# Kernel tuning notes

Measured on AMD Instinct MI355X. Metric: run time of the kernel, lower is better.

Reference implementation:

```python
import math
import numpy as np
import jax, jax.numpy as jnp

LMAX1, LMAX2 = 10, 5
F1, F2 = 20, 40
B_IN, B_L1, B_L2 = 96, 10, 6
ASPECT = 2
BATCH = 32
ACT_CST = math.sqrt(2.0)  # normalize2mom(relu): E[relu(z)^2]=1/2 for z~N(0,1)


def _fact(n):
    return float(math.factorial(n))


def wigner_d_small(l, beta):
    # Wigner small-d matrices, complex-m ordering m=-l..l -> [n, 2l+1, 2l+1]
    beta = np.asarray(beta, dtype=np.float64)
    n = beta.shape[0]
    d = np.zeros((n, 2 * l + 1, 2 * l + 1))
    c, s = np.cos(beta / 2), np.sin(beta / 2)
    for imp, mp in enumerate(range(-l, l + 1)):
        for im, m in enumerate(range(-l, l + 1)):
            pref = math.sqrt(_fact(l + mp) * _fact(l - mp) * _fact(l + m) * _fact(l - m))
            val = np.zeros(n)
            for k in range(max(0, m - mp), min(l + m, l - mp) + 1):
                den = _fact(l + m - k) * _fact(k) * _fact(mp - m + k) * _fact(l - mp - k)
                val += (-1.0) ** (mp - m + k) / den * c ** (2 * l + m - mp - 2 * k) * s ** (mp - m + 2 * k)
            d[:, imp, im] = pref * val
    return d


def U_c2r(l):
    # unitary change of basis complex SH -> real SH, Yr = U @ Yc
    U = np.zeros((2 * l + 1, 2 * l + 1), dtype=np.complex128)
    U[l, l] = 1.0
    sq = 1.0 / math.sqrt(2.0)
    for m in range(1, l + 1):
        cs = (-1.0) ** m
        U[l + m, l + m] = cs * sq
        U[l + m, l - m] = sq
        U[l - m, l + m] = -1j * cs * sq
        U[l - m, l - m] = 1j * sq
    return U


def rot_z_real(l, ang):
    # real-basis rotation about the azimuthal axis -> [n, 2l+1, 2l+1]
    U = U_c2r(l)
    m = np.arange(-l, l + 1)
    ph = np.exp(-1j * np.outer(np.asarray(ang, np.float64), m))
    return np.real(np.einsum('ik,nk,jk->nij', U, ph, U.conj(), optimize=True))


def d_real(l, beta):
    U = U_c2r(l)
    dc = wigner_d_small(l, beta).astype(np.complex128)
    return np.real(np.einsum('ij,njk,lk->nil', U, dc, U.conj(), optimize=True))


def wigner_D_pts(l, a, b, g):
    return np.einsum('nij,njk,nkm->nim', rot_z_real(l, a), d_real(l, b), rot_z_real(l, g), optimize=True)


def flat_wigner_pts(lmax, a, b, g):
    n = len(a)
    return np.concatenate([math.sqrt(2 * l + 1) * wigner_D_pts(l, a, b, g).reshape(n, -1) for l in range(lmax + 1)], -1)


def flat_wigner_grid(lmax, al, be, ga):
    # product grid (alpha x beta x gamma), flattened alpha-major -> [na*nb*ng, sum (2l+1)^2]
    blocks = []
    for l in range(lmax + 1):
        D = np.einsum('aij,bjk,gkm->abgim', rot_z_real(l, al), d_real(l, be), rot_z_real(l, ga), optimize=True)
        blocks.append(math.sqrt(2 * l + 1) * D.reshape(-1, (2 * l + 1) ** 2))
    return np.concatenate(blocks, -1)


def sh_pts(lmax, a, b):
    # component-normalized real SH at points: Y_l = sqrt(2l+1) * D^l(a,b,0)[:, m=0]
    cols = []
    for l in range(lmax + 1):
        M = np.einsum('nij,nj->ni', rot_z_real(l, a), d_real(l, b)[:, :, l], optimize=True)
        cols.append(math.sqrt(2 * l + 1) * M)
    return np.concatenate(cols, -1)


def sh_grid(lmax, al, be):
    # SH on product grid, flattened beta-major to match x.transpose(-1,-2) layout
    cols = []
    for l in range(lmax + 1):
        M = np.einsum('aij,bj->bai', rot_z_real(l, al), d_real(l, be)[:, :, l], optimize=True)
        cols.append(math.sqrt(2 * l + 1) * M.reshape(-1, 2 * l + 1))
    return np.concatenate(cols, -1)


def _so3_grid(res):
    nb, na = 2 * res, 2 * res * ASPECT
    al = 2 * math.pi * np.arange(na) / na
    be = math.pi * (np.arange(nb) + 0.5) / nb
    return al, be, al.copy()


def setup_inputs():
    key = jax.random.key(0)
    k1, k2, k3 = jax.random.split(key, 3)
    # kernel grids (near identity), as in s2/so3_near_identity_grid
    b_s2 = np.arange(1, 4) * (math.pi / 8) / 3
    a_s2 = np.linspace(0, 2 * math.pi, 9)[:-1]
    ga, gb = np.meshgrid(a_s2, b_s2, indexing='ij')
    Yk1 = sh_pts(LMAX1, ga.ravel(), gb.ravel())  # [24, 121]
    a_so3 = np.linspace(0, 2 * math.pi, 8)[:-1]
    g_so3 = np.linspace(-2 * math.pi, 2 * math.pi, 8)
    ga, gb, gg = np.meshgrid(a_so3, b_s2, g_so3, indexing='ij')
    Dk2 = flat_wigner_pts(LMAX2, ga.ravel(), gb.ravel(), gg.ravel())  # [168, 286]
    # FromS2Grid analysis matrix (pinv of band-limited synthesis matrix)
    be = (np.arange(B_IN) + 0.5) / B_IN * math.pi
    al = np.arange(B_IN) / B_IN * 2 * math.pi
    from_s2 = np.linalg.pinv(sh_grid(LMAX1, al, be))  # [121, 9216]
    # SO(3) activation transform matrices
    a1, b1, g1 = _so3_grid(B_L1)
    D1_to = flat_wigner_grid(LMAX1, a1, b1, g1)                     # [32000, 1771]
    F1_from = np.linalg.pinv(flat_wigner_grid(LMAX2, a1, b1, g1))   # [286, 32000]
    a2, b2, g2 = _so3_grid(B_L2)
    D2_to = flat_wigner_grid(LMAX2, a2, b2, g2)                     # [6912, 286]
    F2_from = np.linalg.pinv(flat_wigner_grid(0, a2, b2, g2))       # [1, 6912]
    f32 = lambda v: jnp.asarray(v, dtype=jnp.float32)
    return {
        'x': jax.random.normal(k1, (BATCH, 1, B_IN, B_IN), dtype=jnp.float32),
        'w1': jax.random.normal(k2, (1, F1, Yk1.shape[0]), dtype=jnp.float32),
        'w2': jax.random.normal(k3, (F1, F2, Dk2.shape[0]), dtype=jnp.float32),
        'Yk1': f32(Yk1), 'Dk2': f32(Dk2), 'from_s2': f32(from_s2),
        'D1_to': f32(D1_to), 'F1_from': f32(F1_from),
        'D2_to': f32(D2_to), 'F2_from': f32(F2_from),
    }


def reference(x, w1, w2, Yk1, Dk2, from_s2, D1_to, F1_from, D2_to, F2_from):
    B = x.shape[0]
    # [B,1,alpha,beta] -> [B,1,beta,alpha] -> S2 Fourier coefficients
    c = jnp.einsum('bfg,cg->bfc', jnp.swapaxes(x, -1, -2).reshape(B, 1, -1), from_s2)  # [B,1,121]
    # S2 -> SO(3) convolution (e3nn Linear with SH-built weights)
    psi1 = jnp.einsum('ni,xyn->xyi', Yk1, w1) / math.sqrt(Yk1.shape[0])  # [1,F1,121]
    outs = []
    for l in range(LMAX1 + 1):
        k = 2 * l + 1
        ol = jnp.einsum('bim,ijn->bjnm', c[:, :, l * l:l * l + k], psi1[:, :, l * l:l * l + k])  # fan_in = 1
        outs.append(ol.reshape(B, F1, k * k))
    h = jnp.concatenate(outs, -1)  # [B,F1,1771]
    # SO(3) activation: Fourier -> grid, relu, grid -> Fourier (lmax 10 -> 5)
    g = ACT_CST * jax.nn.relu(jnp.einsum('bfc,gc->bfg', h, D1_to))
    h = jnp.einsum('bfg,cg->bfc', g, F1_from)  # [B,F1,286]
    # SO(3) -> SO(3) convolution (Wigner-D-built weights)
    psi2 = jnp.einsum('nc,xyn->xyc', Dk2, w2) / math.sqrt(Dk2.shape[0])  # [F1,F2,286]
    outs, off = [], 0
    for l in range(LMAX2 + 1):
        k = 2 * l + 1
        xl = h[:, :, off:off + k * k].reshape(B, F1, k, k)       # [B,i,u,m]
        pl = psi2[:, :, off:off + k * k].reshape(F1, F2, k, k)   # [i,j,u,v]
        ol = jnp.einsum('bium,ijuv->bjvm', xl, pl) / math.sqrt(F1 * k)  # fan_in = F1*(2l+1)
        outs.append(ol.reshape(B, F2, k * k))
        off += k * k
    h = jnp.concatenate(outs, -1)  # [B,F2,286]
    # final SO(3) activation lmax 5 -> 0
    g = ACT_CST * jax.nn.relu(jnp.einsum('bfc,gc->bfg', h, D2_to))
    return jnp.einsum('bfg,cg->bfc', g, F2_from)  # [B,F2,1]
```

## Files before the change

kernel.cpp:

```cpp
#include <hip/hip_runtime.h>
#include <hip/hip_bf16.h>
#include <math.h>


#define B_      32
#define F1_     20
#define F2_     40
#define NC1     1771
#define K1P     1792
#define NG1     32000
#define NC2     286
#define K2P     288
#define NG2     6912
#define SQRT2_  1.41421356237309515f
#define RS24    0.20412414523193154f
#define RS168   0.07715167498104595f

typedef unsigned int   uint32;
typedef unsigned short u16;
typedef __attribute__((ext_vector_type(8))) short short8;
typedef __attribute__((ext_vector_type(4))) float f32x4;

#define AS1(p) ((const __attribute__((address_space(1))) void*)(p))
#define AS3(p) ((__attribute__((address_space(3))) void*)(p))

__device__ __forceinline__ u16 f2bf(float f) {
  uint32 u = __float_as_uint(f);
  return (u16)((u + 0x7FFFu + ((u >> 16) & 1u)) >> 16);
}
__device__ __forceinline__ uint32 pack_bf16(float lo, float hi) {
  uint32 a = __float_as_uint(lo), b = __float_as_uint(hi);
  a = (a + 0x7FFFu + ((a >> 16) & 1u)) >> 16;
  b = (b + 0x7FFFu + ((b >> 16) & 1u)) & 0xFFFF0000u;
  return a | b;
}

__device__ __forceinline__ float wave_reduce(float v) {
#pragma unroll
  for (int o = 32; o > 0; o >>= 1) v += __shfl_down(v, o, 64);
  return v;
}


__global__ void k_c(const float* __restrict__ x, const float* __restrict__ fs,
                    float* __restrict__ c) {
  const int ch = blockIdx.x, b = blockIdx.y, tid = threadIdx.x;
  const float* xb = x + b * 9216;
  const float* fr = fs + ch * 9216;
  float s = 0.f;
  for (int g = tid; g < 9216; g += 256) {
    s += xb[(g % 96) * 96 + (g / 96)] * fr[g];
  }
  s = wave_reduce(s);
  __shared__ float red[4];
  if ((tid & 63) == 0) red[tid >> 6] = s;
  __syncthreads();
  if (tid == 0) c[b * 121 + ch] = red[0] + red[1] + red[2] + red[3];
}

__global__ void k_psi1(const float* __restrict__ Yk1, const float* __restrict__ w1,
                       float* __restrict__ psi1) {
  const int j = blockIdx.x, i = threadIdx.x;
  __shared__ float wsm[24];
  if (i < 24) wsm[i] = w1[j * 24 + i];
  __syncthreads();
  if (i < 121) {
    float s = 0.f;
#pragma unroll
    for (int n = 0; n < 24; ++n) s += Yk1[n * 121 + i] * wsm[n];
    psi1[j * 121 + i] = s * RS24;
  }
}

__global__ void k_h(const float* __restrict__ c, const float* __restrict__ psi1,
                    u16* __restrict__ hb) {
  const int j = blockIdx.x, b = blockIdx.y, tid = threadIdx.x;
  __shared__ float cs[121], ps[121];
  if (tid < 121) { cs[tid] = c[b * 121 + tid]; ps[tid] = psi1[j * 121 + tid]; }
  __syncthreads();
  for (int idx = tid; idx < K1P; idx += 256) {
    u16 v = 0;
    if (idx < NC1) {
      int off = 0, l = 0, k = 1;
      while (idx >= off + k * k) { off += k * k; ++l; k += 2; }
      const int r = idx - off, n = r / k, m = r % k;
      v = f2bf(cs[l * l + m] * ps[l * l + n]);
    }
    hb[(size_t)(b * F1_ + j) * K1P + idx] = v;
  }
}


__global__ void k_cvt1(const float* __restrict__ in, uint32* __restrict__ out) {
  const int total = 32000 * 896;
  for (int id = blockIdx.x * 256 + threadIdx.x; id < total; id += gridDim.x * 256) {
    const int r = id / 896, c2 = id % 896, cc = c2 * 2;
    const float* p = in + (size_t)r * NC1 + cc;
    const float lo = (cc < NC1) ? p[0] : 0.f;
    const float hi = (cc + 1 < NC1) ? p[1] : 0.f;
    out[id] = pack_bf16(lo, hi);
  }
}

__global__ void k_cvt2(const float* __restrict__ in, uint32* __restrict__ out) {
  const int total = 286 * 16000;
  for (int id = blockIdx.x * 256 + threadIdx.x; id < total; id += gridDim.x * 256) {
    out[id] = pack_bf16(in[2 * id], in[2 * id + 1]);
  }
}

__global__ void k_cvt3(const float* __restrict__ in, uint32* __restrict__ out) {
  const int total = 6912 * 144;
  for (int id = blockIdx.x * 256 + threadIdx.x; id < total; id += gridDim.x * 256) {
    const int r = id / 144, c2 = id % 144, cc = c2 * 2;
    const float* p = in + (size_t)r * NC2 + cc;
    const float lo = (cc < NC2) ? p[0] : 0.f;
    const float hi = (cc + 1 < NC2) ? p[1] : 0.f;
    out[id] = pack_bf16(lo, hi);
  }
}


__launch_bounds__(256)
__global__ void k_gemm1_v3(const u16* __restrict__ A, const u16* __restrict__ B,
                           u16* __restrict__ C) {
  __shared__ __align__(16) u16 As[128 * 32];
  __shared__ __align__(16) u16 Bs[128 * 32];
  const int bid = blockIdx.x;
  const int g = bid / 40, loc = bid % 40;
  int nt, mt;
  if (g < 31) { nt = g * 8 + (loc & 7); mt = loc >> 3; }
  else        { nt = 248 + (loc & 1);  mt = loc >> 1; }
  const int m0 = mt * 128, n0 = nt * 128;
  const int tid = threadIdx.x;
  const int lane = tid & 63, w = tid >> 6;
  const int wm = w >> 1, wn = w & 1;
  const int q = lane >> 4, r16 = lane & 15;

  f32x4 acc[4][4] = {};
  const u16* ag = A + (size_t)(m0 + (tid >> 2)) * K1P + (tid & 3) * 8;
  const u16* bg = B + (size_t)(n0 + (tid >> 2)) * K1P + (tid & 3) * 8;

  for (int k0 = 0; k0 < K1P; k0 += 32) {
#pragma unroll
    for (int i = 0; i < 2; ++i) {
      __builtin_amdgcn_global_load_lds(AS1(ag + k0 + (size_t)i * 64 * K1P),
                                       AS3((char*)As + i * 4096 + w * 1024), 16, 0, 0);
      __builtin_amdgcn_global_load_lds(AS1(bg + k0 + (size_t)i * 64 * K1P),
                                       AS3((char*)Bs + i * 4096 + w * 1024), 16, 0, 0);
    }
    __syncthreads();
    short8 af[4], bf[4];
#pragma unroll
    for (int mb = 0; mb < 4; ++mb)
      af[mb] = *(const short8*)&As[(wm * 64 + mb * 16 + r16) * 32 + q * 8];
#pragma unroll
    for (int nb = 0; nb < 4; ++nb)
      bf[nb] = *(const short8*)&Bs[(wn * 64 + nb * 16 + r16) * 32 + q * 8];
#pragma unroll
    for (int mb = 0; mb < 4; ++mb)
#pragma unroll
      for (int nb = 0; nb < 4; ++nb)
        acc[mb][nb] = __builtin_amdgcn_mfma_f32_16x16x32_bf16(af[mb], bf[nb], acc[mb][nb], 0, 0, 0);
    __syncthreads();
  }
#pragma unroll
  for (int mb = 0; mb < 4; ++mb) {
#pragma unroll
    for (int nb = 0; nb < 4; ++nb) {
      const int col = n0 + wn * 64 + nb * 16 + r16;
#pragma unroll
      for (int r = 0; r < 4; ++r) {
        const int row = m0 + wm * 64 + mb * 16 + q * 4 + r;
        float v = acc[mb][nb][r];
        v = (v > 0.f) ? v * SQRT2_ : 0.f;
        C[(size_t)row * NG1 + col] = f2bf(v);
      }
    }
  }
}

__launch_bounds__(256)
__global__ void k_gemm2_v3(const u16* __restrict__ A, const u16* __restrict__ B,
                           float* __restrict__ C) {
  __shared__ __align__(16) u16 As[128 * 32];
  __shared__ __align__(16) u16 Bs[128 * 32];
  const int m0 = blockIdx.x * 128, n0 = blockIdx.y * 128;
  const int ks = blockIdx.z * 1600;
  const int tid = threadIdx.x;
  const int lane = tid & 63, w = tid >> 6;
  const int wm = w >> 1, wn = w & 1;
  const int q = lane >> 4, r16 = lane & 15;

  f32x4 acc[4][4] = {};
  const u16* ag = A + (size_t)(m0 + (tid >> 2)) * NG1 + ks + (tid & 3) * 8;
  int rb0 = n0 + (tid >> 2);        if (rb0 > 285) rb0 = 285;
  int rb1 = n0 + (tid >> 2) + 64;   if (rb1 > 285) rb1 = 285;
  const u16* bg0 = B + (size_t)rb0 * NG1 + ks + (tid & 3) * 8;
  const u16* bg1 = B + (size_t)rb1 * NG1 + ks + (tid & 3) * 8;

  for (int kt = 0; kt < 1600; kt += 32) {
#pragma unroll
    for (int i = 0; i < 2; ++i) {
      __builtin_amdgcn_global_load_lds(AS1(ag + kt + (size_t)i * 64 * NG1),
                                       AS3((char*)As + i * 4096 + w * 1024), 16, 0, 0);
    }
    __builtin_amdgcn_global_load_lds(AS1(bg0 + kt), AS3((char*)Bs + w * 1024), 16, 0, 0);
    __builtin_amdgcn_global_load_lds(AS1(bg1 + kt), AS3((char*)Bs + 4096 + w * 1024), 16, 0, 0);
    __syncthreads();
    short8 af[4], bf[4];
#pragma unroll
    for (int mb = 0; mb < 4; ++mb)
      af[mb] = *(const short8*)&As[(wm * 64 + mb * 16 + r16) * 32 + q * 8];
#pragma unroll
    for (int nb = 0; nb < 4; ++nb)
      bf[nb] = *(const short8*)&Bs[(wn * 64 + nb * 16 + r16) * 32 + q * 8];
#pragma unroll
    for (int mb = 0; mb < 4; ++mb)
#pragma unroll
      for (int nb = 0; nb < 4; ++nb)
        acc[mb][nb] = __builtin_amdgcn_mfma_f32_16x16x32_bf16(af[mb], bf[nb], acc[mb][nb], 0, 0, 0);
    __syncthreads();
  }
#pragma unroll
  for (int mb = 0; mb < 4; ++mb) {
#pragma unroll
    for (int nb = 0; nb < 4; ++nb) {
      const int col = n0 + wn * 64 + nb * 16 + r16;
      if (col < NC2) {
#pragma unroll
        for (int r = 0; r < 4; ++r) {
          const int row = m0 + wm * 64 + mb * 16 + q * 4 + r;
          atomicAdd(&C[(size_t)row * NC2 + col], acc[mb][nb][r]);
        }
      }
    }
  }
}

__launch_bounds__(256)
__global__ void k_gemm3_v3(const u16* __restrict__ A, const u16* __restrict__ B,
                           const float* __restrict__ wv, float* __restrict__ out) {
  __shared__ __align__(16) u16 As[128 * 32];
  __shared__ __align__(16) u16 Bs[128 * 32];
  __shared__ float red[128][33];
  const int m0 = blockIdx.x * 128, n0 = blockIdx.y * 128;
  const int tid = threadIdx.x;
  const int lane = tid & 63, w = tid >> 6;
  const int wm = w >> 1, wn = w & 1;
  const int q = lane >> 4, r16 = lane & 15;

  f32x4 acc[4][4] = {};
  const u16* ag = A + (size_t)(m0 + (tid >> 2)) * K2P + (tid & 3) * 8;
  const u16* bg = B + (size_t)(n0 + (tid >> 2)) * K2P + (tid & 3) * 8;

  for (int k0 = 0; k0 < K2P; k0 += 32) {
#pragma unroll
    for (int i = 0; i < 2; ++i) {
      __builtin_amdgcn_global_load_lds(AS1(ag + k0 + (size_t)i * 64 * K2P),
                                       AS3((char*)As + i * 4096 + w * 1024), 16, 0, 0);
      __builtin_amdgcn_global_load_lds(AS1(bg + k0 + (size_t)i * 64 * K2P),
                                       AS3((char*)Bs + i * 4096 + w * 1024), 16, 0, 0);
    }
    __syncthreads();
    short8 af[4], bf[4];
#pragma unroll
    for (int mb = 0; mb < 4; ++mb)
      af[mb] = *(const short8*)&As[(wm * 64 + mb * 16 + r16) * 32 + q * 8];
#pragma unroll
    for (int nb = 0; nb < 4; ++nb)
      bf[nb] = *(const short8*)&Bs[(wn * 64 + nb * 16 + r16) * 32 + q * 8];
#pragma unroll
    for (int mb = 0; mb < 4; ++mb)
#pragma unroll
      for (int nb = 0; nb < 4; ++nb)
        acc[mb][nb] = __builtin_amdgcn_mfma_f32_16x16x32_bf16(af[mb], bf[nb], acc[mb][nb], 0, 0, 0);
    __syncthreads();
  }
  float wvv[4];
#pragma unroll
  for (int nb = 0; nb < 4; ++nb) wvv[nb] = wv[n0 + wn * 64 + nb * 16 + r16];
#pragma unroll
  for (int mb = 0; mb < 4; ++mb) {
#pragma unroll
    for (int r = 0; r < 4; ++r) {
      const int rowl = wm * 64 + mb * 16 + q * 4 + r;
      float t = 0.f;
#pragma unroll
      for (int nb = 0; nb < 4; ++nb) {
        float v = acc[mb][nb][r];
        v = (v > 0.f) ? v : 0.f;
        t += v * wvv[nb];
      }
      red[rowl][wn * 16 + r16] = t;
    }
  }
  __syncthreads();
  if (tid < 128) {
    float s = 0.f;
#pragma unroll
    for (int cc = 0; cc < 32; ++cc) s += red[tid][cc];
    atomicAdd(&out[m0 + tid], s * SQRT2_);
  }
}


__launch_bounds__(256)
__global__ void k_gemm1_mfma(const u16* __restrict__ A, const float* __restrict__ Bf,
                             u16* __restrict__ C) {
  __shared__ __align__(16) u16 As[128 * 32];
  __shared__ __align__(16) u16 Bs[128 * 32];
  const int tid = threadIdx.x;
  const int lane = tid & 63, w = tid >> 6;
  const int wm = w >> 1, wn = w & 1;
  const int q = lane >> 4, r16 = lane & 15;
  const int m0 = blockIdx.x * 128, n0 = blockIdx.y * 128;

  f32x4 acc[4][4] = {};
  const u16* ag = A + (size_t)(m0 + (tid >> 2)) * K1P + (tid & 3) * 8;

  for (int k0 = 0; k0 < K1P; k0 += 32) {
#pragma unroll
    for (int i = 0; i < 2; ++i) {
      __builtin_amdgcn_global_load_lds(AS1(ag + k0 + (size_t)i * 64 * K1P),
                                       AS3((char*)As + i * 4096 + w * 1024), 16, 0, 0);
    }
#pragma unroll
    for (int i = 0; i < 8; ++i) {
      const int p = i * 256 + tid;
      const int row = p >> 4, c2 = (p & 15) * 2;
      const int kk = k0 + c2;
      const float* bp = Bf + (size_t)(n0 + row) * NC1 + kk;
      const float lo = (kk < NC1) ? bp[0] : 0.f;
      const float hi = (kk + 1 < NC1) ? bp[1] : 0.f;
      ((uint32*)Bs)[row * 16 + (p & 15)] = pack_bf16(lo, hi);
    }
    __syncthreads();
    short8 af[4], bf[4];
#pragma unroll
    for (int mb = 0; mb < 4; ++mb)
      af[mb] = *(const short8*)&As[(wm * 64 + mb * 16 + r16) * 32 + q * 8];
#pragma unroll
    for (int nb = 0; nb < 4; ++nb)
      bf[nb] = *(const short8*)&Bs[(wn * 64 + nb * 16 + r16) * 32 + q * 8];
#pragma unroll
    for (int mb = 0; mb < 4; ++mb)
#pragma unroll
      for (int nb = 0; nb < 4; ++nb)
        acc[mb][nb] = __builtin_amdgcn_mfma_f32_16x16x32_bf16(af[mb], bf[nb], acc[mb][nb], 0, 0, 0);
    __syncthreads();
  }
#pragma unroll
  for (int mb = 0; mb < 4; ++mb) {
#pragma unroll
    for (int nb = 0; nb < 4; ++nb) {
      const int col = n0 + wn * 64 + nb * 16 + r16;
#pragma unroll
      for (int r = 0; r < 4; ++r) {
        const int row = m0 + wm * 64 + mb * 16 + q * 4 + r;
        float v = acc[mb][nb][r];
        v = (v > 0.f) ? v * SQRT2_ : 0.f;
        C[(size_t)row * NG1 + col] = f2bf(v);
      }
    }
  }
}

__launch_bounds__(256)
__global__ void k_gemm2_mfma(const u16* __restrict__ A, const float* __restrict__ Bf,
                             float* __restrict__ C) {
  __shared__ __align__(16) u16 As[128 * 32];
  __shared__ __align__(16) u16 Bs[128 * 32];
  const int tid = threadIdx.x;
  const int lane = tid & 63, w = tid >> 6;
  const int wm = w >> 1, wn = w & 1;
  const int q = lane >> 4, r16 = lane & 15;
  const int m0 = blockIdx.x * 128, n0 = blockIdx.y * 128;
  const int ks = blockIdx.z * 1600;

  f32x4 acc[4][4] = {};
  const u16* ag = A + (size_t)(m0 + (tid >> 2)) * NG1 + ks + (tid & 3) * 8;

  for (int kt = 0; kt < 1600; kt += 32) {
#pragma unroll
    for (int i = 0; i < 2; ++i) {
      __builtin_amdgcn_global_load_lds(AS1(ag + kt + (size_t)i * 64 * NG1),
                                       AS3((char*)As + i * 4096 + w * 1024), 16, 0, 0);
    }
#pragma unroll
    for (int i = 0; i < 4; ++i) {
      const int idx = i * 256 + tid;
      const int row = idx >> 3, c4 = (idx & 7) * 4;
      const int n = n0 + row;
      float4 v = make_float4(0.f, 0.f, 0.f, 0.f);
      if (n < NC2) v = *(const float4*)(Bf + (size_t)n * NG1 + ks + kt + c4);
      ((uint32*)Bs)[row * 16 + (idx & 7) * 2]     = pack_bf16(v.x, v.y);
      ((uint32*)Bs)[row * 16 + (idx & 7) * 2 + 1] = pack_bf16(v.z, v.w);
    }
    __syncthreads();
    short8 af[4], bf[4];
#pragma unroll
    for (int mb = 0; mb < 4; ++mb)
      af[mb] = *(const short8*)&As[(wm * 64 + mb * 16 + r16) * 32 + q * 8];
#pragma unroll
    for (int nb = 0; nb < 4; ++nb)
      bf[nb] = *(const short8*)&Bs[(wn * 64 + nb * 16 + r16) * 32 + q * 8];
#pragma unroll
    for (int mb = 0; mb < 4; ++mb)
#pragma unroll
      for (int nb = 0; nb < 4; ++nb)
        acc[mb][nb] = __builtin_amdgcn_mfma_f32_16x16x32_bf16(af[mb], bf[nb], acc[mb][nb], 0, 0, 0);
    __syncthreads();
  }
#pragma unroll
  for (int mb = 0; mb < 4; ++mb) {
#pragma unroll
    for (int nb = 0; nb < 4; ++nb) {
      const int col = n0 + wn * 64 + nb * 16 + r16;
      if (col < NC2) {
#pragma unroll
        for (int r = 0; r < 4; ++r) {
          const int row = m0 + wm * 64 + mb * 16 + q * 4 + r;
          atomicAdd(&C[(size_t)row * NC2 + col], acc[mb][nb][r]);
        }
      }
    }
  }
}


__global__ void k_psi2(const float* __restrict__ Dk2, const float* __restrict__ w2,
                       float* __restrict__ psi2) {
  const int blk = blockIdx.x, tid = threadIdx.x;
  __shared__ float w2s[168];
  if (tid < 168) w2s[tid] = w2[blk * 168 + tid];
  __syncthreads();
  for (int cc = tid; cc < NC2; cc += 256) {
    float s = 0.f;
    for (int n = 0; n < 168; ++n) s += Dk2[n * NC2 + cc] * w2s[n];
    psi2[blk * NC2 + cc] = s * RS168;
  }
}

__global__ void k_step7(const float* __restrict__ h2, const float* __restrict__ psi2,
                        u16* __restrict__ h3b) {
  const int j = blockIdx.x, b = blockIdx.y, tid = threadIdx.x;
  __shared__ float sh[20 * 286];
  __shared__ float sp[20 * 286];
  for (int e = tid; e < 20 * 286; e += 256) {
    const int i = e / 286, cc = e % 286;
    sh[e] = h2[(b * F1_ + i) * NC2 + cc];
    sp[e] = psi2[(i * F2_ + j) * NC2 + cc];
  }
  __syncthreads();
  for (int cidx = tid; cidx < K2P; cidx += 256) {
    u16 ov = 0;
    if (cidx < NC2) {
      int off = 0, l = 0, k = 1;
      while (cidx >= off + k * k) { off += k * k; ++l; k += 2; }
      const int r = cidx - off, v = r / k, m = r % k;
      float acc = 0.f;
      for (int i = 0; i < 20; ++i) {
        const float* hbp = &sh[i * 286 + off];
        const float* pb = &sp[i * 286 + off];
        for (int u = 0; u < k; ++u) acc += hbp[u * k + m] * pb[u * k + v];
      }
      ov = f2bf(acc * rsqrtf(20.f * (float)k));
    }
    h3b[(size_t)(b * F2_ + j) * K2P + cidx] = ov;
  }
}


extern "C" void kernel_launch(void* const* d_in, const int* in_sizes, int n_in,
                              void* d_out, int out_size, void* d_ws, size_t ws_size,
                              hipStream_t stream) {
  const float* x       = (const float*)d_in[0];
  const float* w1      = (const float*)d_in[1];
  const float* w2      = (const float*)d_in[2];
  const float* Yk1     = (const float*)d_in[3];
  const float* Dk2     = (const float*)d_in[4];
  const float* from_s2 = (const float*)d_in[5];
  const float* D1_to   = (const float*)d_in[6];
  const float* F1_from = (const float*)d_in[7];
  const float* D2_to   = (const float*)d_in[8];
  const float* F2_from = (const float*)d_in[9];
  float* out = (float*)d_out;

  float* ws = (float*)d_ws;
  float* c    = ws + 0;
  float* psi1 = ws + 3872;
  float* h2   = ws + 6292;
  float* psi2 = ws + 189332;
  u16*   h3b  = (u16*)(ws + 418132);
  u16*   hb   = (u16*)(ws + 602452);
  u16*   g    = (u16*)(ws + 1175892);
  u16*   D2bf = (u16*)(ws + 11415892);
  u16*   F1bf = (u16*)(ws + 12411220);
  u16*   D1bf = (u16*)(ws + 16987220);
  const size_t BIG_NEED = (size_t)45659220 * 4;
  const bool big = ws_size >= BIG_NEED;

  k_c   <<<dim3(121, 32), 256, 0, stream>>>(x, from_s2, c);
  k_psi1<<<dim3(20),      128, 0, stream>>>(Yk1, w1, psi1);
  k_h   <<<dim3(20, 32),  256, 0, stream>>>(c, psi1, hb);
  k_cvt3<<<dim3(1024),    256, 0, stream>>>(D2_to, (uint32*)D2bf);

  if (big) {
    k_cvt1<<<dim3(8192), 256, 0, stream>>>(D1_to, (uint32*)D1bf);
    k_cvt2<<<dim3(4096), 256, 0, stream>>>(F1_from, (uint32*)F1bf);
    k_gemm1_v3<<<dim3(1250), 256, 0, stream>>>(hb, D1bf, g);
    hipMemsetAsync(h2, 0, (size_t)640 * 286 * sizeof(float), stream);
    k_gemm2_v3<<<dim3(5, 3, 20), 256, 0, stream>>>(g, F1bf, h2);
  } else {
    k_gemm1_mfma<<<dim3(5, 250), 256, 0, stream>>>(hb, D1_to, g);
    hipMemsetAsync(h2, 0, (size_t)640 * 286 * sizeof(float), stream);
    k_gemm2_mfma<<<dim3(5, 3, 20), 256, 0, stream>>>(g, F1_from, h2);
  }

  k_psi2 <<<dim3(800),    256, 0, stream>>>(Dk2, w2, psi2);
  k_step7<<<dim3(40, 32), 256, 0, stream>>>(h2, psi2, h3b);

  hipMemsetAsync(out, 0, (size_t)1280 * sizeof(float), stream);
  k_gemm3_v3<<<dim3(10, 54), 256, 0, stream>>>(h3b, D2bf, F2_from, out);
}
```

Before: 776.1 us.

## Merge prep kernels into one launch and triple-buffer the first GEMM

New measurement: 676.8 us. 1.15x faster.

```diff
diff --git a/kernel.cpp b/kernel.cpp
--- a/kernel.cpp
+++ b/kernel.cpp
@@ -24,6 +24,9 @@
 #define AS1(p) ((const __attribute__((address_space(1))) void*)(p))
 #define AS3(p) ((__attribute__((address_space(3))) void*)(p))
 
+#define WAITCNT_VM8 0x0F78
+#define WAITCNT_VM0 0x0F70
+
 __device__ __forceinline__ u16 f2bf(float f) {
   uint32 u = __float_as_uint(f);
   return (u16)((u + 0x7FFFu + ((u >> 16) & 1u)) >> 16);
@@ -41,35 +44,123 @@
   return v;
 }
 
-
-__global__ void k_c(const float* __restrict__ x, const float* __restrict__ fs,
-                    float* __restrict__ c) {
+#define PREP_BLOCKS (8192 + 2048 + 512 + 800 + 288 + 20 + 184)
+
+__global__ void k_prep(const float* __restrict__ D1, const float* __restrict__ F1,
+                       const float* __restrict__ D2, const float* __restrict__ Yk1,
+                       const float* __restrict__ w1, const float* __restrict__ Dk2,
+                       const float* __restrict__ w2, const float* __restrict__ x,
+                       uint32* __restrict__ D1bf, uint32* __restrict__ F1bf,
+                       uint32* __restrict__ D2bf, float* __restrict__ psi1,
+                       float* __restrict__ psi2, float* __restrict__ xt,
+                       float* __restrict__ h2z, float* __restrict__ outz) {
+  __shared__ float smem[1056];
+  int bid = blockIdx.x;
+  const int tid = threadIdx.x;
+  if (bid < 8192) {
+    const int total = 32000 * 896;
+    for (int id = bid * 256 + tid; id < total; id += 8192 * 256) {
+      const int r = id / 896, c2 = id % 896, cc = c2 * 2;
+      const float* p = D1 + (size_t)r * NC1 + cc;
+      const float lo = (cc < NC1) ? p[0] : 0.f;
+      const float hi = (cc + 1 < NC1) ? p[1] : 0.f;
+      D1bf[id] = pack_bf16(lo, hi);
+    }
+    return;
+  }
+  bid -= 8192;
+  if (bid < 2048) {
+    const int total = 286 * 16000;
+    for (int id = bid * 256 + tid; id < total; id += 2048 * 256) {
+      F1bf[id] = pack_bf16(F1[2 * id], F1[2 * id + 1]);
+    }
+    return;
+  }
+  bid -= 2048;
+  if (bid < 512) {
+    const int total = 6912 * 144;
+    for (int id = bid * 256 + tid; id < total; id += 512 * 256) {
+      const int r = id / 144, c2 = id % 144, cc = c2 * 2;
+      const float* p = D2 + (size_t)r * NC2 + cc;
+      const float lo = (cc < NC2) ? p[0] : 0.f;
+      const float hi = (cc + 1 < NC2) ? p[1] : 0.f;
+      D2bf[id] = pack_bf16(lo, hi);
+    }
+    return;
+  }
+  bid -= 512;
+  if (bid < 800) {
+    float* w2s = smem;
+    if (tid < 168) w2s[tid] = w2[bid * 168 + tid];
+    __syncthreads();
+    for (int cc = tid; cc < NC2; cc += 256) {
+      float s = 0.f;
+      for (int n = 0; n < 168; ++n) s += Dk2[n * NC2 + cc] * w2s[n];
+      psi2[bid * NC2 + cc] = s * RS168;
+    }
+    return;
+  }
+  bid -= 800;
+  if (bid < 288) {
+    float (*t)[33] = (float(*)[33])smem;
+    const int b = bid / 9, r9 = bid % 9, i0 = (r9 % 3) * 32, j0 = (r9 / 3) * 32;
+    const int tx = tid & 31, ty0 = tid >> 5;
+    const float* xb = x + b * 9216;
+    float* xtb = xt + b * 9216;
+#pragma unroll
+    for (int r = 0; r < 4; ++r) {
+      const int ty = ty0 + r * 8;
+      t[ty][tx] = xb[(i0 + ty) * 96 + j0 + tx];
+    }
+    __syncthreads();
+#pragma unroll
+    for (int r = 0; r < 4; ++r) {
+      const int ty = ty0 + r * 8;
+      xtb[(j0 + ty) * 96 + i0 + tx] = t[tx][ty];
+    }
+    return;
+  }
+  bid -= 288;
+  if (bid < 20) {
+    float* wsm = smem;
+    if (tid < 24) wsm[tid] = w1[bid * 24 + tid];
+    __syncthreads();
+    if (tid < 121) {
+      float s = 0.f;
+#pragma unroll
+      for (int n = 0; n < 24; ++n) s += Yk1[n * 121 + tid] * wsm[n];
+      psi1[bid * 121 + tid] = s * RS24;
+    }
+    return;
+  }
+  bid -= 20;
+  {
+    int id = bid * 256 + tid;
+    if (id < 45760) {
+      ((float4*)h2z)[id] = make_float4(0.f, 0.f, 0.f, 0.f);
+    } else {
+      id -= 45760;
+      if (id < 1280) outz[id] = 0.f;
+    }
+  }
+}
+
+__global__ void k_c2(const float* __restrict__ xt, const float* __restrict__ fs,
+                     float* __restrict__ c) {
   const int ch = blockIdx.x, b = blockIdx.y, tid = threadIdx.x;
-  const float* xb = x + b * 9216;
-  const float* fr = fs + ch * 9216;
+  const float4* xb = (const float4*)(xt + b * 9216);
+  const float4* fr = (const float4*)(fs + ch * 9216);
   float s = 0.f;
-  for (int g = tid; g < 9216; g += 256) {
-    s += xb[(g % 96) * 96 + (g / 96)] * fr[g];
+#pragma unroll 3
+  for (int g = tid; g < 2304; g += 256) {
+    const float4 a = xb[g], d = fr[g];
+    s += a.x * d.x + a.y * d.y + a.z * d.z + a.w * d.w;
   }
   s = wave_reduce(s);
   __shared__ float red[4];
   if ((tid & 63) == 0) red[tid >> 6] = s;
   __syncthreads();
   if (tid == 0) c[b * 121 + ch] = red[0] + red[1] + red[2] + red[3];
-}
-
-__global__ void k_psi1(const float* __restrict__ Yk1, const float* __restrict__ w1,
-                       float* __restrict__ psi1) {
-  const int j = blockIdx.x, i = threadIdx.x;
-  __shared__ float wsm[24];
-  if (i < 24) wsm[i] = w1[j * 24 + i];
-  __syncthreads();
-  if (i < 121) {
-    float s = 0.f;
-#pragma unroll
-    for (int n = 0; n < 24; ++n) s += Yk1[n * 121 + i] * wsm[n];
-    psi1[j * 121 + i] = s * RS24;
-  }
 }
 
 __global__ void k_h(const float* __restrict__ c, const float* __restrict__ psi1,
@@ -90,85 +181,77 @@
   }
 }
 
-
-__global__ void k_cvt1(const float* __restrict__ in, uint32* __restrict__ out) {
-  const int total = 32000 * 896;
-  for (int id = blockIdx.x * 256 + threadIdx.x; id < total; id += gridDim.x * 256) {
-    const int r = id / 896, c2 = id % 896, cc = c2 * 2;
-    const float* p = in + (size_t)r * NC1 + cc;
-    const float lo = (cc < NC1) ? p[0] : 0.f;
-    const float hi = (cc + 1 < NC1) ? p[1] : 0.f;
-    out[id] = pack_bf16(lo, hi);
-  }
-}
-
-__global__ void k_cvt2(const float* __restrict__ in, uint32* __restrict__ out) {
-  const int total = 286 * 16000;
-  for (int id = blockIdx.x * 256 + threadIdx.x; id < total; id += gridDim.x * 256) {
-    out[id] = pack_bf16(in[2 * id], in[2 * id + 1]);
-  }
-}
-
-__global__ void k_cvt3(const float* __restrict__ in, uint32* __restrict__ out) {
-  const int total = 6912 * 144;
-  for (int id = blockIdx.x * 256 + threadIdx.x; id < total; id += gridDim.x * 256) {
-    const int r = id / 144, c2 = id % 144, cc = c2 * 2;
-    const float* p = in + (size_t)r * NC2 + cc;
-    const float lo = (cc < NC2) ? p[0] : 0.f;
-    const float hi = (cc + 1 < NC2) ? p[1] : 0.f;
-    out[id] = pack_bf16(lo, hi);
-  }
-}
-
-
-__launch_bounds__(256)
-__global__ void k_gemm1_v3(const u16* __restrict__ A, const u16* __restrict__ B,
+__launch_bounds__(128)
+__global__ void k_gemm1_v6(const u16* __restrict__ A, const u16* __restrict__ B,
                            u16* __restrict__ C) {
-  __shared__ __align__(16) u16 As[128 * 32];
-  __shared__ __align__(16) u16 Bs[128 * 32];
+  __shared__ __align__(16) u16 As0[128 * 32], As1[128 * 32], As2[128 * 32];
+  __shared__ __align__(16) u16 Bs0[128 * 32], Bs1[128 * 32], Bs2[128 * 32];
   const int bid = blockIdx.x;
-  const int g = bid / 40, loc = bid % 40;
+  const int gg = bid / 40, loc = bid % 40;
   int nt, mt;
-  if (g < 31) { nt = g * 8 + (loc & 7); mt = loc >> 3; }
-  else        { nt = 248 + (loc & 1);  mt = loc >> 1; }
+  if (gg < 31) { nt = gg * 8 + (loc & 7); mt = loc >> 3; }
+  else         { nt = 248 + (loc & 1);   mt = loc >> 1; }
   const int m0 = mt * 128, n0 = nt * 128;
   const int tid = threadIdx.x;
-  const int lane = tid & 63, w = tid >> 6;
-  const int wm = w >> 1, wn = w & 1;
+  const int lane = tid & 63, wm = tid >> 6;
   const int q = lane >> 4, r16 = lane & 15;
 
-  f32x4 acc[4][4] = {};
   const u16* ag = A + (size_t)(m0 + (tid >> 2)) * K1P + (tid & 3) * 8;
   const u16* bg = B + (size_t)(n0 + (tid >> 2)) * K1P + (tid & 3) * 8;
 
-  for (int k0 = 0; k0 < K1P; k0 += 32) {
-#pragma unroll
-    for (int i = 0; i < 2; ++i) {
-      __builtin_amdgcn_global_load_lds(AS1(ag + k0 + (size_t)i * 64 * K1P),
-                                       AS3((char*)As + i * 4096 + w * 1024), 16, 0, 0);
-      __builtin_amdgcn_global_load_lds(AS1(bg + k0 + (size_t)i * 64 * K1P),
-                                       AS3((char*)Bs + i * 4096 + w * 1024), 16, 0, 0);
-    }
-    __syncthreads();
-    short8 af[4], bf[4];
-#pragma unroll
-    for (int mb = 0; mb < 4; ++mb)
-      af[mb] = *(const short8*)&As[(wm * 64 + mb * 16 + r16) * 32 + q * 8];
-#pragma unroll
-    for (int nb = 0; nb < 4; ++nb)
-      bf[nb] = *(const short8*)&Bs[(wn * 64 + nb * 16 + r16) * 32 + q * 8];
-#pragma unroll
-    for (int mb = 0; mb < 4; ++mb)
-#pragma unroll
-      for (int nb = 0; nb < 4; ++nb)
-        acc[mb][nb] = __builtin_amdgcn_mfma_f32_16x16x32_bf16(af[mb], bf[nb], acc[mb][nb], 0, 0, 0);
-    __syncthreads();
-  }
+#define G1_ISSUE(kk, Asb, Bsb)                                                     \
+  {                                                                                \
+    _Pragma("unroll")                                                              \
+    for (int i = 0; i < 4; ++i) {                                                  \
+      __builtin_amdgcn_global_load_lds(AS1(ag + (kk) * 32 + (size_t)i * 32 * K1P), \
+          AS3((char*)(Asb) + i * 2048 + wm * 1024), 16, 0, 0);                     \
+      __builtin_amdgcn_global_load_lds(AS1(bg + (kk) * 32 + (size_t)i * 32 * K1P), \
+          AS3((char*)(Bsb) + i * 2048 + wm * 1024), 16, 0, 0);                     \
+    }                                                                              \
+  }
+
+#define G1_COMPUTE(Asb, Bsb)                                                       \
+  {                                                                                \
+    short8 af[4], bq[8];                                                           \
+    _Pragma("unroll")                                                              \
+    for (int mb = 0; mb < 4; ++mb)                                                 \
+      af[mb] = *(const short8*)&(Asb)[(wm * 64 + mb * 16 + r16) * 32 + q * 8];     \
+    _Pragma("unroll")                                                              \
+    for (int nb = 0; nb < 8; ++nb)                                                 \
+      bq[nb] = *(const short8*)&(Bsb)[(nb * 16 + r16) * 32 + q * 8];               \
+    _Pragma("unroll")                                                              \
+    for (int mb = 0; mb < 4; ++mb)                                                 \
+      _Pragma("unroll")                                                            \
+      for (int nb = 0; nb < 8; ++nb)                                               \
+        acc[mb][nb] = __builtin_amdgcn_mfma_f32_16x16x32_bf16(af[mb], bq[nb],      \
+                                                              acc[mb][nb], 0, 0, 0); \
+  }
+
+#define G1_STAGE(kk, wt, AsR, BsR, AsI, BsI)        \
+  {                                                 \
+    __builtin_amdgcn_s_waitcnt(wt);                 \
+    __builtin_amdgcn_s_barrier();                   \
+    asm volatile("" ::: "memory");                  \
+    if ((kk) + 2 < 56) G1_ISSUE((kk) + 2, AsI, BsI) \
+    G1_COMPUTE(AsR, BsR)                            \
+  }
+
+  f32x4 acc[4][8] = {};
+  G1_ISSUE(0, As0, Bs0)
+  G1_ISSUE(1, As1, Bs1)
+  for (int k = 0; k < 54; k += 3) {
+    G1_STAGE(k,     WAITCNT_VM8, As0, Bs0, As2, Bs2)
+    G1_STAGE(k + 1, WAITCNT_VM8, As1, Bs1, As0, Bs0)
+    G1_STAGE(k + 2, WAITCNT_VM8, As2, Bs2, As1, Bs1)
+  }
+  G1_STAGE(54, WAITCNT_VM8, As0, Bs0, As2, Bs2)
+  G1_STAGE(55, WAITCNT_VM0, As1, Bs1, As0, Bs0)
+
 #pragma unroll
   for (int mb = 0; mb < 4; ++mb) {
 #pragma unroll
-    for (int nb = 0; nb < 4; ++nb) {
-      const int col = n0 + wn * 64 + nb * 16 + r16;
+    for (int nb = 0; nb < 8; ++nb) {
+      const int col = n0 + nb * 16 + r16;
 #pragma unroll
       for (int r = 0; r < 4; ++r) {
         const int row = m0 + wm * 64 + mb * 16 + q * 4 + r;
@@ -178,6 +261,9 @@
       }
     }
   }
+#undef G1_ISSUE
+#undef G1_COMPUTE
+#undef G1_STAGE
 }
 
 __launch_bounds__(256)
@@ -208,18 +294,18 @@
     __builtin_amdgcn_global_load_lds(AS1(bg0 + kt), AS3((char*)Bs + w * 1024), 16, 0, 0);
     __builtin_amdgcn_global_load_lds(AS1(bg1 + kt), AS3((char*)Bs + 4096 + w * 1024), 16, 0, 0);
     __syncthreads();
-    short8 af[4], bf[4];
+    short8 af[4], bq[4];
 #pragma unroll
     for (int mb = 0; mb < 4; ++mb)
       af[mb] = *(const short8*)&As[(wm * 64 + mb * 16 + r16) * 32 + q * 8];
 #pragma unroll
     for (int nb = 0; nb < 4; ++nb)
-      bf[nb] = *(const short8*)&Bs[(wn * 64 + nb * 16 + r16) * 32 + q * 8];
+      bq[nb] = *(const short8*)&Bs[(wn * 64 + nb * 16 + r16) * 32 + q * 8];
 #pragma unroll
     for (int mb = 0; mb < 4; ++mb)
 #pragma unroll
       for (int nb = 0; nb < 4; ++nb)
-        acc[mb][nb] = __builtin_amdgcn_mfma_f32_16x16x32_bf16(af[mb], bf[nb], acc[mb][nb], 0, 0, 0);
+        acc[mb][nb] = __builtin_amdgcn_mfma_f32_16x16x32_bf16(af[mb], bq[nb], acc[mb][nb], 0, 0, 0);
     __syncthreads();
   }
 #pragma unroll
@@ -263,18 +349,18 @@
                                        AS3((char*)Bs + i * 4096 + w * 1024), 16, 0, 0);
     }
     __syncthreads();
-    short8 af[4], bf[4];
+    short8 af[4], bq[4];
 #pragma unroll
     for (int mb = 0; mb < 4; ++mb)
       af[mb] = *(const short8*)&As[(wm * 64 + mb * 16 + r16) * 32 + q * 8];
 #pragma unroll
     for (int nb = 0; nb < 4; ++nb)
-      bf[nb] = *(const short8*)&Bs[(wn * 64 + nb * 16 + r16) * 32 + q * 8];
+      bq[nb] = *(const short8*)&Bs[(wn * 64 + nb * 16 + r16) * 32 + q * 8];
 #pragma unroll
     for (int mb = 0; mb < 4; ++mb)
 #pragma unroll
       for (int nb = 0; nb < 4; ++nb)
-        acc[mb][nb] = __builtin_amdgcn_mfma_f32_16x16x32_bf16(af[mb], bf[nb], acc[mb][nb], 0, 0, 0);
+        acc[mb][nb] = __builtin_amdgcn_mfma_f32_16x16x32_bf16(af[mb], bq[nb], acc[mb][nb], 0, 0, 0);
     __syncthreads();
   }
   float wvv[4];
@@ -304,143 +390,6 @@
   }
 }
 
-
-__launch_bounds__(256)
-__global__ void k_gemm1_mfma(const u16* __restrict__ A, const float* __restrict__ Bf,
-                             u16* __restrict__ C) {
-  __shared__ __align__(16) u16 As[128 * 32];
-  __shared__ __align__(16) u16 Bs[128 * 32];
-  const int tid = threadIdx.x;
-  const int lane = tid & 63, w = tid >> 6;
-  const int wm = w >> 1, wn = w & 1;
-  const int q = lane >> 4, r16 = lane & 15;
-  const int m0 = blockIdx.x * 128, n0 = blockIdx.y * 128;
-
-  f32x4 acc[4][4] = {};
-  const u16* ag = A + (size_t)(m0 + (tid >> 2)) * K1P + (tid & 3) * 8;
-
-  for (int k0 = 0; k0 < K1P; k0 += 32) {
-#pragma unroll
-    for (int i = 0; i < 2; ++i) {
-      __builtin_amdgcn_global_load_lds(AS1(ag + k0 + (size_t)i * 64 * K1P),
-                                       AS3((char*)As + i * 4096 + w * 1024), 16, 0, 0);
-    }
-#pragma unroll
-    for (int i = 0; i < 8; ++i) {
-      const int p = i * 256 + tid;
-      const int row = p >> 4, c2 = (p & 15) * 2;
-      const int kk = k0 + c2;
-      const float* bp = Bf + (size_t)(n0 + row) * NC1 + kk;
-      const float lo = (kk < NC1) ? bp[0] : 0.f;
-      const float hi = (kk + 1 < NC1) ? bp[1] : 0.f;
-      ((uint32*)Bs)[row * 16 + (p & 15)] = pack_bf16(lo, hi);
-    }
-    __syncthreads();
-    short8 af[4], bf[4];
-#pragma unroll
-    for (int mb = 0; mb < 4; ++mb)
-      af[mb] = *(const short8*)&As[(wm * 64 + mb * 16 + r16) * 32 + q * 8];
-#pragma unroll
-    for (int nb = 0; nb < 4; ++nb)
-      bf[nb] = *(const short8*)&Bs[(wn * 64 + nb * 16 + r16) * 32 + q * 8];
-#pragma unroll
-    for (int mb = 0; mb < 4; ++mb)
-#pragma unroll
-      for (int nb = 0; nb < 4; ++nb)
-        acc[mb][nb] = __builtin_amdgcn_mfma_f32_16x16x32_bf16(af[mb], bf[nb], acc[mb][nb], 0, 0, 0);
-    __syncthreads();
-  }
-#pragma unroll
-  for (int mb = 0; mb < 4; ++mb) {
-#pragma unroll
-    for (int nb = 0; nb < 4; ++nb) {
-      const int col = n0 + wn * 64 + nb * 16 + r16;
-#pragma unroll
-      for (int r = 0; r < 4; ++r) {
-        const int row = m0 + wm * 64 + mb * 16 + q * 4 + r;
-        float v = acc[mb][nb][r];
-        v = (v > 0.f) ? v * SQRT2_ : 0.f;
-        C[(size_t)row * NG1 + col] = f2bf(v);
-      }
-    }
-  }
-}
-
-__launch_bounds__(256)
-__global__ void k_gemm2_mfma(const u16* __restrict__ A, const float* __restrict__ Bf,
-                             float* __restrict__ C) {
-  __shared__ __align__(16) u16 As[128 * 32];
-  __shared__ __align__(16) u16 Bs[128 * 32];
-  const int tid = threadIdx.x;
-  const int lane = tid & 63, w = tid >> 6;
-  const int wm = w >> 1, wn = w & 1;
-  const int q = lane >> 4, r16 = lane & 15;
-  const int m0 = blockIdx.x * 128, n0 = blockIdx.y * 128;
-  const int ks = blockIdx.z * 1600;
-
-  f32x4 acc[4][4] = {};
-  const u16* ag = A + (size_t)(m0 + (tid >> 2)) * NG1 + ks + (tid & 3) * 8;
-
-  for (int kt = 0; kt < 1600; kt += 32) {
-#pragma unroll
-    for (int i = 0; i < 2; ++i) {
-      __builtin_amdgcn_global_load_lds(AS1(ag + kt + (size_t)i * 64 * NG1),
-                                       AS3((char*)As + i * 4096 + w * 1024), 16, 0, 0);
-    }
-#pragma unroll
-    for (int i = 0; i < 4; ++i) {
-      const int idx = i * 256 + tid;
-      const int row = idx >> 3, c4 = (idx & 7) * 4;
-      const int n = n0 + row;
-      float4 v = make_float4(0.f, 0.f, 0.f, 0.f);
-      if (n < NC2) v = *(const float4*)(Bf + (size_t)n * NG1 + ks + kt + c4);
-      ((uint32*)Bs)[row * 16 + (idx & 7) * 2]     = pack_bf16(v.x, v.y);
-      ((uint32*)Bs)[row * 16 + (idx & 7) * 2 + 1] = pack_bf16(v.z, v.w);
-    }
-    __syncthreads();
-    short8 af[4], bf[4];
-#pragma unroll
-    for (int mb = 0; mb < 4; ++mb)
-      af[mb] = *(const short8*)&As[(wm * 64 + mb * 16 + r16) * 32 + q * 8];
-#pragma unroll
-    for (int nb = 0; nb < 4; ++nb)
-      bf[nb] = *(const short8*)&Bs[(wn * 64 + nb * 16 + r16) * 32 + q * 8];
-#pragma unroll
-    for (int mb = 0; mb < 4; ++mb)
-#pragma unroll
-      for (int nb = 0; nb < 4; ++nb)
-        acc[mb][nb] = __builtin_amdgcn_mfma_f32_16x16x32_bf16(af[mb], bf[nb], acc[mb][nb], 0, 0, 0);
-    __syncthreads();
-  }
-#pragma unroll
-  for (int mb = 0; mb < 4; ++mb) {
-#pragma unroll
-    for (int nb = 0; nb < 4; ++nb) {
-      const int col = n0 + wn * 64 + nb * 16 + r16;
-      if (col < NC2) {
-#pragma unroll
-        for (int r = 0; r < 4; ++r) {
-          const int row = m0 + wm * 64 + mb * 16 + q * 4 + r;
-          atomicAdd(&C[(size_t)row * NC2 + col], acc[mb][nb][r]);
-        }
-      }
-    }
-  }
-}
-
-
-__global__ void k_psi2(const float* __restrict__ Dk2, const float* __restrict__ w2,
-                       float* __restrict__ psi2) {
-  const int blk = blockIdx.x, tid = threadIdx.x;
-  __shared__ float w2s[168];
-  if (tid < 168) w2s[tid] = w2[blk * 168 + tid];
-  __syncthreads();
-  for (int cc = tid; cc < NC2; cc += 256) {
-    float s = 0.f;
-    for (int n = 0; n < 168; ++n) s += Dk2[n * NC2 + cc] * w2s[n];
-    psi2[blk * NC2 + cc] = s * RS168;
-  }
-}
 
 __global__ void k_step7(const float* __restrict__ h2, const float* __restrict__ psi2,
                         u16* __restrict__ h3b) {
@@ -472,6 +421,184 @@
 }
 
 
+__global__ void k_c(const float* __restrict__ x, const float* __restrict__ fs,
+                    float* __restrict__ c) {
+  const int ch = blockIdx.x, b = blockIdx.y, tid = threadIdx.x;
+  const float* xb = x + b * 9216;
+  const float* fr = fs + ch * 9216;
+  float s = 0.f;
+  for (int g = tid; g < 9216; g += 256) {
+    s += xb[(g % 96) * 96 + (g / 96)] * fr[g];
+  }
+  s = wave_reduce(s);
+  __shared__ float red[4];
+  if ((tid & 63) == 0) red[tid >> 6] = s;
+  __syncthreads();
+  if (tid == 0) c[b * 121 + ch] = red[0] + red[1] + red[2] + red[3];
+}
+
+__global__ void k_psi1(const float* __restrict__ Yk1, const float* __restrict__ w1,
+                       float* __restrict__ psi1) {
+  const int j = blockIdx.x, i = threadIdx.x;
+  __shared__ float wsm[24];
+  if (i < 24) wsm[i] = w1[j * 24 + i];
+  __syncthreads();
+  if (i < 121) {
+    float s = 0.f;
+#pragma unroll
+    for (int n = 0; n < 24; ++n) s += Yk1[n * 121 + i] * wsm[n];
+    psi1[j * 121 + i] = s * RS24;
+  }
+}
+
+__global__ void k_psi2(const float* __restrict__ Dk2, const float* __restrict__ w2,
+                       float* __restrict__ psi2) {
+  const int blk = blockIdx.x, tid = threadIdx.x;
+  __shared__ float w2s[168];
+  if (tid < 168) w2s[tid] = w2[blk * 168 + tid];
+  __syncthreads();
+  for (int cc = tid; cc < NC2; cc += 256) {
+    float s = 0.f;
+    for (int n = 0; n < 168; ++n) s += Dk2[n * NC2 + cc] * w2s[n];
+    psi2[blk * NC2 + cc] = s * RS168;
+  }
+}
+
+__global__ void k_cvt3(const float* __restrict__ in, uint32* __restrict__ out) {
+  const int total = 6912 * 144;
+  for (int id = blockIdx.x * 256 + threadIdx.x; id < total; id += gridDim.x * 256) {
+    const int r = id / 144, c2 = id % 144, cc = c2 * 2;
+    const float* p = in + (size_t)r * NC2 + cc;
+    const float lo = (cc < NC2) ? p[0] : 0.f;
+    const float hi = (cc + 1 < NC2) ? p[1] : 0.f;
+    out[id] = pack_bf16(lo, hi);
+  }
+}
+
+__launch_bounds__(256)
+__global__ void k_gemm1_mfma(const u16* __restrict__ A, const float* __restrict__ Bf,
+                             u16* __restrict__ C) {
+  __shared__ __align__(16) u16 As[128 * 32];
+  __shared__ __align__(16) u16 Bs[128 * 32];
+  const int tid = threadIdx.x;
+  const int lane = tid & 63, w = tid >> 6;
+  const int wm = w >> 1, wn = w & 1;
+  const int q = lane >> 4, r16 = lane & 15;
+  const int m0 = blockIdx.x * 128, n0 = blockIdx.y * 128;
+
+  f32x4 acc[4][4] = {};
+  const u16* ag = A + (size_t)(m0 + (tid >> 2)) * K1P + (tid & 3) * 8;
+
+  for (int k0 = 0; k0 < K1P; k0 += 32) {
+#pragma unroll
+    for (int i = 0; i < 2; ++i) {
+      __builtin_amdgcn_global_load_lds(AS1(ag + k0 + (size_t)i * 64 * K1P),
+                                       AS3((char*)As + i * 4096 + w * 1024), 16, 0, 0);
+    }
+#pragma unroll
+    for (int i = 0; i < 8; ++i) {
+      const int p = i * 256 + tid;
+      const int row = p >> 4, c2 = (p & 15) * 2;
+      const int kk = k0 + c2;
+      const float* bpp = Bf + (size_t)(n0 + row) * NC1 + kk;
+      const float lo = (kk < NC1) ? bpp[0] : 0.f;
+      const float hi = (kk + 1 < NC1) ? bpp[1] : 0.f;
+      ((uint32*)Bs)[row * 16 + (p & 15)] = pack_bf16(lo, hi);
+    }
+    __syncthreads();
+    short8 af[4], bq[4];
+#pragma unroll
+    for (int mb = 0; mb < 4; ++mb)
+      af[mb] = *(const short8*)&As[(wm * 64 + mb * 16 + r16) * 32 + q * 8];
+#pragma unroll
+    for (int nb = 0; nb < 4; ++nb)
+      bq[nb] = *(const short8*)&Bs[(wn * 64 + nb * 16 + r16) * 32 + q * 8];
+#pragma unroll
+    for (int mb = 0; mb < 4; ++mb)
+#pragma unroll
+      for (int nb = 0; nb < 4; ++nb)
+        acc[mb][nb] = __builtin_amdgcn_mfma_f32_16x16x32_bf16(af[mb], bq[nb], acc[mb][nb], 0, 0, 0);
+    __syncthreads();
+  }
+#pragma unroll
+  for (int mb = 0; mb < 4; ++mb) {
+#pragma unroll
+    for (int nb = 0; nb < 4; ++nb) {
+      const int col = n0 + wn * 64 + nb * 16 + r16;
+#pragma unroll
+      for (int r = 0; r < 4; ++r) {
+        const int row = m0 + wm * 64 + mb * 16 + q * 4 + r;
+        float v = acc[mb][nb][r];
+        v = (v > 0.f) ? v * SQRT2_ : 0.f;
+        C[(size_t)row * NG1 + col] = f2bf(v);
+      }
+    }
+  }
+}
+
+__launch_bounds__(256)
+__global__ void k_gemm2_mfma(const u16* __restrict__ A, const float* __restrict__ Bf,
+                             float* __restrict__ C) {
+  __shared__ __align__(16) u16 As[128 * 32];
+  __shared__ __align__(16) u16 Bs[128 * 32];
+  const int tid = threadIdx.x;
+  const int lane = tid & 63, w = tid >> 6;
+  const int wm = w >> 1, wn = w & 1;
+  const int q = lane >> 4, r16 = lane & 15;
+  const int m0 = blockIdx.x * 128, n0 = blockIdx.y * 128;
+  const int ks = blockIdx.z * 1600;
+
+  f32x4 acc[4][4] = {};
+  const u16* ag = A + (size_t)(m0 + (tid >> 2)) * NG1 + ks + (tid & 3) * 8;
+
+  for (int kt = 0; kt < 1600; kt += 32) {
+#pragma unroll
+    for (int i = 0; i < 2; ++i) {
+      __builtin_amdgcn_global_load_lds(AS1(ag + kt + (size_t)i * 64 * NG1),
+                                       AS3((char*)As + i * 4096 + w * 1024), 16, 0, 0);
+    }
+#pragma unroll
+    for (int i = 0; i < 4; ++i) {
+      const int idx = i * 256 + tid;
+      const int row = idx >> 3, c4 = (idx & 7) * 4;
+      const int n = n0 + row;
+      float4 v = make_float4(0.f, 0.f, 0.f, 0.f);
+      if (n < NC2) v = *(const float4*)(Bf + (size_t)n * NG1 + ks + kt + c4);
+      ((uint32*)Bs)[row * 16 + (idx & 7) * 2]     = pack_bf16(v.x, v.y);
+      ((uint32*)Bs)[row * 16 + (idx & 7) * 2 + 1] = pack_bf16(v.z, v.w);
+    }
+    __syncthreads();
+    short8 af[4], bq[4];
+#pragma unroll
+    for (int mb = 0; mb < 4; ++mb)
+      af[mb] = *(const short8*)&As[(wm * 64 + mb * 16 + r16) * 32 + q * 8];
+#pragma unroll
+    for (int nb = 0; nb < 4; ++nb)
+      bq[nb] = *(const short8*)&Bs[(wn * 64 + nb * 16 + r16) * 32 + q * 8];
+#pragma unroll
+    for (int mb = 0; mb < 4; ++mb)
+#pragma unroll
+      for (int nb = 0; nb < 4; ++nb)
+        acc[mb][nb] = __builtin_amdgcn_mfma_f32_16x16x32_bf16(af[mb], bq[nb], acc[mb][nb], 0, 0, 0);
+    __syncthreads();
+  }
+#pragma unroll
+  for (int mb = 0; mb < 4; ++mb) {
+#pragma unroll
+    for (int nb = 0; nb < 4; ++nb) {
+      const int col = n0 + wn * 64 + nb * 16 + r16;
+      if (col < NC2) {
+#pragma unroll
+        for (int r = 0; r < 4; ++r) {
+          const int row = m0 + wm * 64 + mb * 16 + q * 4 + r;
+          atomicAdd(&C[(size_t)row * NC2 + col], acc[mb][nb][r]);
+        }
+      }
+    }
+  }
+}
+
+
 extern "C" void kernel_launch(void* const* d_in, const int* in_sizes, int n_in,
                               void* d_out, int out_size, void* d_ws, size_t ws_size,
                               hipStream_t stream) {
@@ -498,29 +625,31 @@
   u16*   D2bf = (u16*)(ws + 11415892);
   u16*   F1bf = (u16*)(ws + 12411220);
   u16*   D1bf = (u16*)(ws + 16987220);
-  const size_t BIG_NEED = (size_t)45659220 * 4;
-  const bool big = ws_size >= BIG_NEED;
-
-  k_c   <<<dim3(121, 32), 256, 0, stream>>>(x, from_s2, c);
-  k_psi1<<<dim3(20),      128, 0, stream>>>(Yk1, w1, psi1);
-  k_h   <<<dim3(20, 32),  256, 0, stream>>>(c, psi1, hb);
-  k_cvt3<<<dim3(1024),    256, 0, stream>>>(D2_to, (uint32*)D2bf);
+  float* x_t  = ws + 45659220;
+  const size_t NEED = (size_t)45954132 * 4;
+  const bool big = ws_size >= NEED;
 
   if (big) {
-    k_cvt1<<<dim3(8192), 256, 0, stream>>>(D1_to, (uint32*)D1bf);
-    k_cvt2<<<dim3(4096), 256, 0, stream>>>(F1_from, (uint32*)F1bf);
-    k_gemm1_v3<<<dim3(1250), 256, 0, stream>>>(hb, D1bf, g);
-    hipMemsetAsync(h2, 0, (size_t)640 * 286 * sizeof(float), stream);
+    k_prep<<<dim3(PREP_BLOCKS), 256, 0, stream>>>(
+        D1_to, F1_from, D2_to, Yk1, w1, Dk2, w2, x,
+        (uint32*)D1bf, (uint32*)F1bf, (uint32*)D2bf, psi1, psi2, x_t, h2, out);
+    k_c2<<<dim3(121, 32), 256, 0, stream>>>(x_t, from_s2, c);
+    k_h <<<dim3(20, 32),  256, 0, stream>>>(c, psi1, hb);
+    k_gemm1_v6<<<dim3(1250), 128, 0, stream>>>(hb, D1bf, g);
     k_gemm2_v3<<<dim3(5, 3, 20), 256, 0, stream>>>(g, F1bf, h2);
+    k_step7<<<dim3(40, 32), 256, 0, stream>>>(h2, psi2, h3b);
+    k_gemm3_v3<<<dim3(10, 54), 256, 0, stream>>>(h3b, D2bf, F2_from, out);
   } else {
+    k_c   <<<dim3(121, 32), 256, 0, stream>>>(x, from_s2, c);
+    k_psi1<<<dim3(20),      128, 0, stream>>>(Yk1, w1, psi1);
+    k_h   <<<dim3(20, 32),  256, 0, stream>>>(c, psi1, hb);
+    k_cvt3<<<dim3(1024),    256, 0, stream>>>(D2_to, (uint32*)D2bf);
     k_gemm1_mfma<<<dim3(5, 250), 256, 0, stream>>>(hb, D1_to, g);
     hipMemsetAsync(h2, 0, (size_t)640 * 286 * sizeof(float), stream);
     k_gemm2_mfma<<<dim3(5, 3, 20), 256, 0, stream>>>(g, F1_from, h2);
-  }
-
-  k_psi2 <<<dim3(800),    256, 0, stream>>>(Dk2, w2, psi2);
-  k_step7<<<dim3(40, 32), 256, 0, stream>>>(h2, psi2, h3b);
-
-  hipMemsetAsync(out, 0, (size_t)1280 * sizeof(float), stream);
-  k_gemm3_v3<<<dim3(10, 54), 256, 0, stream>>>(h3b, D2bf, F2_from, out);
-}
+    k_psi2 <<<dim3(800),    256, 0, stream>>>(Dk2, w2, psi2);
+    k_step7<<<dim3(40, 32), 256, 0, stream>>>(h2, psi2, h3b);
+    hipMemsetAsync(out, 0, (size_t)1280 * sizeof(float), stream);
+    k_gemm3_v3<<<dim3(10, 54), 256, 0, stream>>>(h3b, D2bf, F2_from, out);
+  }
+}
```
